# Optimization experiments

Hardware: AMD Instinct MI355X
Metric: run time of the kernel (lower is better)

## Reference

```python
import jax, jax.numpy as jnp
import numpy as np

N_NODES = 20000
N_REL = 200
DIM = 128
N_EDGES = 200000
N_TIMES = 8


def setup_inputs() -> dict:
    key = jax.random.key(0)
    ks = jax.random.split(key, 12)
    s = 1.0 / np.sqrt(DIM)
    return {
        "edge_index": jax.random.randint(ks[0], (2, N_EDGES), 0, N_NODES),
        "edge_type": jax.random.randint(ks[1], (N_EDGES,), 0, N_REL),
        "edge_time": jax.random.randint(ks[2], (N_EDGES,), 0, N_TIMES),
        "edge_weight": jax.random.uniform(ks[3], (N_EDGES,), dtype=jnp.float32),
        "node_emb": jax.random.normal(ks[4], (N_NODES, DIM), dtype=jnp.float32),
        "rel_emb": jax.random.normal(ks[5], (N_REL, DIM), dtype=jnp.float32),
        "W_enc": jax.random.normal(ks[6], (DIM, DIM), dtype=jnp.float32) * s,
        "Wz": jax.random.normal(ks[7], (DIM, DIM), dtype=jnp.float32) * s,
        "Uz": jax.random.normal(ks[8], (DIM, DIM), dtype=jnp.float32) * s,
        "Wh": jax.random.normal(ks[9], (DIM, DIM), dtype=jnp.float32) * s,
        "Uh": jax.random.normal(ks[10], (DIM, DIM), dtype=jnp.float32) * s,
        "bz": jnp.zeros((DIM,), dtype=jnp.float32),
        "bh": jnp.zeros((DIM,), dtype=jnp.float32),
        "num_times": N_TIMES,
    }


def reference(edge_index, edge_type, edge_time, edge_weight,
              node_emb, rel_emb, W_enc, Wz, Uz, Wh, Uh, bz, bh, num_times):
    # TemporalEncoder.forward: loop over sorted unique timestamps; per-step
    # masked-edge GNN encode (R-GCN lite) then gated SSM cell; state detached.
    src, dst = edge_index[0], edge_index[1]
    rel_e = rel_emb[edge_type]          # [E, D] gather (constant across steps)
    src_e = node_emb[src]               # [E, D]
    n_nodes = node_emb.shape[0]

    def step(state, t):
        m = (edge_time == t).astype(edge_weight.dtype)       # [E]
        msg = src_e * rel_e * (edge_weight * m)[:, None]     # [E, D]
        agg = jax.ops.segment_sum(msg, dst, num_segments=n_nodes)  # [N, D]
        h = jnp.tanh(agg @ W_enc)                            # base_encoder output
        z = jax.nn.sigmoid(h @ Wz + state @ Uz + bz)
        cand = jnp.tanh(h @ Wh + state @ Uh + bh)
        new_state = (1.0 - z) * state + z * cand             # ssm.cell
        return jax.lax.stop_gradient(new_state), new_state   # state.detach()

    state0 = jnp.zeros_like(node_emb)
    _, outs = jax.lax.scan(step, state0, jnp.arange(num_times))
    return outs[-1]  # last_out, shape [N, D]
```

## Files before the change

kernel.cpp:

```cpp
#include <hip/hip_runtime.h>

#define N_NODES 20000
#define N_REL 200
#define N_EDGES 200000
#define DIM 128
#define T_STEPS 8
#define N_TILES (N_NODES / 16)
#define KEYS (N_NODES * T_STEPS)
#define SCAN_N (KEYS + 1)
#define SCAN_BLKS ((SCAN_N + 1023) / 1024)

typedef short short8 __attribute__((ext_vector_type(8)));
typedef float f32x4 __attribute__((ext_vector_type(4)));

static __device__ __forceinline__ unsigned short f2bf(float f) {
  union { float f; unsigned u; } v; v.f = f;
  unsigned r = v.u + 0x7fffu + ((v.u >> 16) & 1u);
  return (unsigned short)(r >> 16);
}
static __device__ __forceinline__ unsigned cvt_pk_bf16(float lo, float hi) {
  unsigned r;
  asm("v_cvt_pk_bf16_f32 %0, %1, %2" : "=v"(r) : "v"(lo), "v"(hi));
  return r;
}
static __device__ __forceinline__ float fast_tanh(float x) {
  float e = __expf(2.f * x);
  return 1.f - 2.f / (e + 1.f);
}
static __device__ __forceinline__ float fast_sig(float x) {
  return 1.f / (1.f + __expf(-x));
}

__global__ void repack5(const float* __restrict__ w0,
                        const float* __restrict__ w1,
                        const float* __restrict__ w2,
                        const float* __restrict__ w3,
                        const float* __restrict__ w4,
                        unsigned short* __restrict__ pack) {
  int i = blockIdx.x * blockDim.x + threadIdx.x;
  if (i >= 5 * 16384) return;
  int m = i >> 14, r = i & 16383;
  int j = r & 7, lane = (r >> 3) & 63, ks = (r >> 9) & 3, nt = (r >> 11) & 7;
  int n = nt * 16 + (lane & 15);
  int k = ks * 32 + (lane >> 4) * 8 + j;
  const float* w = (m == 0) ? w0 : (m == 1) ? w1 : (m == 2) ? w2
                 : (m == 3) ? w3 : w4;
  pack[i] = f2bf(w[k * DIM + n]);
}

__global__ void hist_k(const int* __restrict__ dst, const int* __restrict__ etime,
                       int* __restrict__ counts) {
  int i = blockIdx.x * blockDim.x + threadIdx.x;
  if (i >= N_EDGES) return;
  atomicAdd(&counts[dst[i] * T_STEPS + etime[i]], 1);
}

__global__ void scan1_k(const int* __restrict__ counts,
                        int* __restrict__ base, int* __restrict__ bsum) {
  __shared__ int ls[256];
  int tid = threadIdx.x;
  int i0 = blockIdx.x * 1024 + tid * 4;
  int v[4], ts = 0;
#pragma unroll
  for (int r = 0; r < 4; r++) {
    v[r] = (i0 + r < SCAN_N) ? counts[i0 + r] : 0;
    ts += v[r];
  }
  ls[tid] = ts; __syncthreads();
#pragma unroll
  for (int off = 1; off < 256; off <<= 1) {
    int x = (tid >= off) ? ls[tid - off] : 0;
    __syncthreads(); ls[tid] += x; __syncthreads();
  }
  int run = ls[tid] - ts;
  if (tid == 255) bsum[blockIdx.x] = ls[255];
#pragma unroll
  for (int r = 0; r < 4; r++) {
    if (i0 + r < SCAN_N) base[i0 + r] = run;
    run += v[r];
  }
}

__global__ void scan2_k(int* __restrict__ bsum) {
  __shared__ int ls[256];
  int tid = threadIdx.x;
  int v = (tid < SCAN_BLKS) ? bsum[tid] : 0;
  ls[tid] = v; __syncthreads();
#pragma unroll
  for (int off = 1; off < 256; off <<= 1) {
    int x = (tid >= off) ? ls[tid - off] : 0;
    __syncthreads(); ls[tid] += x; __syncthreads();
  }
  if (tid < SCAN_BLKS) bsum[tid] = ls[tid] - v;
}

__global__ void scan3_k(int* __restrict__ base, const int* __restrict__ bsum) {
  int i = blockIdx.x * blockDim.x + threadIdx.x;
  if (i < SCAN_N) base[i] += bsum[i >> 10];
}

__global__ void fill_k(const int* __restrict__ src, const int* __restrict__ dst,
                       const int* __restrict__ etype, const int* __restrict__ etime,
                       const float* __restrict__ ew,
                       const int* __restrict__ base, int* __restrict__ cursor,
                       unsigned* __restrict__ epack, float* __restrict__ sw) {
  int i = blockIdx.x * blockDim.x + threadIdx.x;
  if (i >= N_EDGES) return;
  int key = dst[i] * T_STEPS + etime[i];
  int pos = base[key] + atomicAdd(&cursor[key], 1);
  epack[pos] = (unsigned)src[i] | ((unsigned)etype[i] << 15);
  sw[pos] = ew[i];
}

__global__ void gather_k(const int* __restrict__ base,
                         const unsigned* __restrict__ epack,
                         const float* __restrict__ sw,
                         const float* __restrict__ nemb,
                         const float* __restrict__ remb,
                         unsigned short* __restrict__ aggb) {
  int lane = threadIdx.x & 63;
  int node = (blockIdx.x * blockDim.x + threadIdx.x) >> 6;
  const int* b = base + node * T_STEPS;
  int i = b[0];
#pragma unroll
  for (int tt = 0; tt < T_STEPS; tt++) {
    int e1 = b[tt + 1];
    float ax = 0.f, ay = 0.f;
    for (; i < e1; i++) {
      unsigned u = epack[i];
      float w = sw[i];
      int s = u & 0x7fff, rt = u >> 15;
      float2 sv = ((const float2*)(nemb + (size_t)s * DIM))[lane];
      float2 rv = ((const float2*)(remb + (size_t)rt * DIM))[lane];
      ax += sv.x * rv.x * w;
      ay += sv.y * rv.y * w;
    }
    ((unsigned*)(aggb + ((size_t)tt * N_NODES + node) * DIM))[lane] =
        cvt_pk_bf16(ax, ay);
  }
}

__launch_bounds__(512, 4)
__global__ void fused_recur(const unsigned short* __restrict__ aggb,
                            const unsigned short* __restrict__ pack,
                            const float* __restrict__ bz,
                            const float* __restrict__ bh,
                            float* __restrict__ out) {
  __shared__ unsigned short Hb[2][16 * 136];
  __shared__ unsigned short Sb[2][16 * 136];
  int lane = threadIdx.x & 63;
  int nt = threadIdx.x >> 6;
  int tile = blockIdx.x;
  int q = lane >> 4, l15 = lane & 15;
  int row0 = tile * 16;

  unsigned hpk[T_STEPS][2];
  {
    short8 wenc[4];
#pragma unroll
    for (int ks = 0; ks < 4; ks++)
      wenc[ks] = *(const short8*)(pack + ((nt * 4 + ks) * 64 + lane) * 8);
#pragma unroll
    for (int t = 0; t < T_STEPS; t++) {
      f32x4 acch = (f32x4){0.f, 0.f, 0.f, 0.f};
#pragma unroll
      for (int ks = 0; ks < 4; ks++) {
        short8 aA = *(const short8*)(aggb +
            ((size_t)t * N_NODES + row0 + l15) * DIM + ks * 32 + q * 8);
        acch = __builtin_amdgcn_mfma_f32_16x16x32_bf16(aA, wenc[ks], acch, 0, 0, 0);
      }
      hpk[t][0] = cvt_pk_bf16(fast_tanh(acch[0]), fast_tanh(acch[1]));
      hpk[t][1] = cvt_pk_bf16(fast_tanh(acch[2]), fast_tanh(acch[3]));
    }
  }

  short8 wz[4], uz[4], wh[4], uh[4];
#pragma unroll
  for (int ks = 0; ks < 4; ks++) {
    int fo = ((nt * 4 + ks) * 64 + lane) * 8;
    wz[ks] = *(const short8*)(pack + 16384 * 1 + fo);
    uz[ks] = *(const short8*)(pack + 16384 * 2 + fo);
    wh[ks] = *(const short8*)(pack + 16384 * 3 + fo);
    uh[ks] = *(const short8*)(pack + 16384 * 4 + fo);
  }
  float bzv = bz[nt * 16 + l15];
  float bhv = bh[nt * 16 + l15];

  f32x4 stC = (f32x4){0.f, 0.f, 0.f, 0.f};
  int c = nt * 16 + l15;

#pragma unroll
  for (int t = 0; t < T_STEPS; t++) {
    unsigned short* hB = Hb[t & 1];
    unsigned short* sB = Sb[t & 1];
    unsigned s01 = cvt_pk_bf16(stC[0], stC[1]);
    unsigned s23 = cvt_pk_bf16(stC[2], stC[3]);
    hB[(q * 4 + 0) * 136 + c] = (unsigned short)hpk[t][0];
    hB[(q * 4 + 1) * 136 + c] = (unsigned short)(hpk[t][0] >> 16);
    hB[(q * 4 + 2) * 136 + c] = (unsigned short)hpk[t][1];
    hB[(q * 4 + 3) * 136 + c] = (unsigned short)(hpk[t][1] >> 16);
    sB[(q * 4 + 0) * 136 + c] = (unsigned short)s01;
    sB[(q * 4 + 1) * 136 + c] = (unsigned short)(s01 >> 16);
    sB[(q * 4 + 2) * 136 + c] = (unsigned short)s23;
    sB[(q * 4 + 3) * 136 + c] = (unsigned short)(s23 >> 16);
    __syncthreads();

    f32x4 accz = (f32x4){bzv, bzv, bzv, bzv};
    f32x4 accc = (f32x4){bhv, bhv, bhv, bhv};
#pragma unroll
    for (int ks = 0; ks < 4; ks++) {
      short8 hA = *(const short8*)&hB[l15 * 136 + ks * 32 + q * 8];
      short8 sA = *(const short8*)&sB[l15 * 136 + ks * 32 + q * 8];
      accz = __builtin_amdgcn_mfma_f32_16x16x32_bf16(hA, wz[ks], accz, 0, 0, 0);
      accz = __builtin_amdgcn_mfma_f32_16x16x32_bf16(sA, uz[ks], accz, 0, 0, 0);
      accc = __builtin_amdgcn_mfma_f32_16x16x32_bf16(hA, wh[ks], accc, 0, 0, 0);
      accc = __builtin_amdgcn_mfma_f32_16x16x32_bf16(sA, uh[ks], accc, 0, 0, 0);
    }
#pragma unroll
    for (int r = 0; r < 4; r++) {
      float z = fast_sig(accz[r]);
      float cc = fast_tanh(accc[r]);
      stC[r] = (1.f - z) * stC[r] + z * cc;
    }
  }

#pragma unroll
  for (int r = 0; r < 4; r++)
    out[(size_t)(row0 + q * 4 + r) * DIM + nt * 16 + l15] = stC[r];
}

extern "C" void kernel_launch(void* const* d_in, const int* in_sizes, int n_in,
                              void* d_out, int out_size, void* d_ws, size_t ws_size,
                              hipStream_t stream) {
  const int* eidx  = (const int*)d_in[0];
  const int* src   = eidx;
  const int* dst   = eidx + N_EDGES;
  const int* etype = (const int*)d_in[1];
  const int* etime = (const int*)d_in[2];
  const float* ew   = (const float*)d_in[3];
  const float* nemb = (const float*)d_in[4];
  const float* remb = (const float*)d_in[5];
  const float* Wenc = (const float*)d_in[6];
  const float* Wz   = (const float*)d_in[7];
  const float* Uz   = (const float*)d_in[8];
  const float* Wh   = (const float*)d_in[9];
  const float* Uh   = (const float*)d_in[10];
  const float* bz   = (const float*)d_in[11];
  const float* bh   = (const float*)d_in[12];

  unsigned short* aggb = (unsigned short*)d_ws;
  int* counts = (int*)(aggb + (size_t)T_STEPS * N_NODES * DIM);
  int* cursor = counts + SCAN_N;
  int* bsum   = cursor + KEYS;
  int* base   = bsum + 256;
  unsigned* epack = (unsigned*)(base + SCAN_N);
  float* sw   = (float*)(epack + N_EDGES);
  unsigned short* pack = (unsigned short*)(sw + N_EDGES);
  float* outp = (float*)d_out;

  hipMemsetAsync(counts, 0, (size_t)(SCAN_N + KEYS) * sizeof(int), stream);
  repack5<<<(5 * 16384 + 255) / 256, 256, 0, stream>>>(Wenc, Wz, Uz, Wh, Uh, pack);
  hist_k<<<(N_EDGES + 255) / 256, 256, 0, stream>>>(dst, etime, counts);
  scan1_k<<<SCAN_BLKS, 256, 0, stream>>>(counts, base, bsum);
  scan2_k<<<1, 256, 0, stream>>>(bsum);
  scan3_k<<<(SCAN_N + 255) / 256, 256, 0, stream>>>(base, bsum);
  fill_k<<<(N_EDGES + 255) / 256, 256, 0, stream>>>(src, dst, etype, etime, ew,
                                                    base, cursor, epack, sw);
  gather_k<<<N_NODES / 4, 256, 0, stream>>>(base, epack, sw, nemb, remb, aggb);
  fused_recur<<<N_TILES, 512, 0, stream>>>(aggb, pack, bz, bh, outp);
}
```

Measured before the change: 226.1 us.

## Give each wave a full node tile in recurrence; pack edge index and weight

The fused recurrence kernel now assigns one 16-row tile per wave, with each wave computing all 8 column tiles. Weights are streamed from global/L2 on every step instead of being held in registers, and state lives in registers as 8x4 floats per lane. Per-wave XOR-swizzled LDS scratch replaces the block-wide shared buffers, which removes __syncthreads, and the first step skips the state matmuls. Edge source/type and weight are packed into one uint2 so each edge needs a single load. The trade-off is repeated weight fetches and higher register pressure in exchange for no block barriers.

```diff
diff --git a/kernel.cpp b/kernel.cpp
--- a/kernel.cpp
+++ b/kernel.cpp
@@ -9,6 +9,8 @@
 #define KEYS (N_NODES * T_STEPS)
 #define SCAN_N (KEYS + 1)
 #define SCAN_BLKS ((SCAN_N + 1023) / 1024)
+#define TILE_WAVES 4
+#define FUSE_BLKS ((N_TILES + TILE_WAVES - 1) / TILE_WAVES)
 
 typedef short short8 __attribute__((ext_vector_type(8)));
 typedef float f32x4 __attribute__((ext_vector_type(4)));
@@ -103,18 +105,19 @@
                        const int* __restrict__ etype, const int* __restrict__ etime,
                        const float* __restrict__ ew,
                        const int* __restrict__ base, int* __restrict__ cursor,
-                       unsigned* __restrict__ epack, float* __restrict__ sw) {
+                       uint2* __restrict__ ep2) {
   int i = blockIdx.x * blockDim.x + threadIdx.x;
   if (i >= N_EDGES) return;
   int key = dst[i] * T_STEPS + etime[i];
   int pos = base[key] + atomicAdd(&cursor[key], 1);
-  epack[pos] = (unsigned)src[i] | ((unsigned)etype[i] << 15);
-  sw[pos] = ew[i];
+  uint2 e;
+  e.x = (unsigned)src[i] | ((unsigned)etype[i] << 15);
+  e.y = __float_as_uint(ew[i]);
+  ep2[pos] = e;
 }
 
 __global__ void gather_k(const int* __restrict__ base,
-                         const unsigned* __restrict__ epack,
-                         const float* __restrict__ sw,
+                         const uint2* __restrict__ ep2,
                          const float* __restrict__ nemb,
                          const float* __restrict__ remb,
                          unsigned short* __restrict__ aggb) {
@@ -127,9 +130,9 @@
     int e1 = b[tt + 1];
     float ax = 0.f, ay = 0.f;
     for (; i < e1; i++) {
-      unsigned u = epack[i];
-      float w = sw[i];
-      int s = u & 0x7fff, rt = u >> 15;
+      uint2 e = ep2[i];
+      float w = __uint_as_float(e.y);
+      int s = e.x & 0x7fff, rt = e.x >> 15;
       float2 sv = ((const float2*)(nemb + (size_t)s * DIM))[lane];
       float2 rv = ((const float2*)(remb + (size_t)rt * DIM))[lane];
       ax += sv.x * rv.x * w;
@@ -140,93 +143,118 @@
   }
 }
 
-__launch_bounds__(512, 4)
+__launch_bounds__(256, 2)
 __global__ void fused_recur(const unsigned short* __restrict__ aggb,
                             const unsigned short* __restrict__ pack,
                             const float* __restrict__ bz,
                             const float* __restrict__ bh,
                             float* __restrict__ out) {
-  __shared__ unsigned short Hb[2][16 * 136];
-  __shared__ unsigned short Sb[2][16 * 136];
+  __shared__ unsigned short scr[TILE_WAVES][2][16 * 128];
   int lane = threadIdx.x & 63;
-  int nt = threadIdx.x >> 6;
-  int tile = blockIdx.x;
+  int wv = threadIdx.x >> 6;
+  int tile = blockIdx.x * TILE_WAVES + wv;
+  if (tile >= N_TILES) return;
   int q = lane >> 4, l15 = lane & 15;
+  int x3 = l15 & 3;
   int row0 = tile * 16;
-
-  unsigned hpk[T_STEPS][2];
-  {
-    short8 wenc[4];
+  unsigned short* hS = &scr[wv][0][0];
+  unsigned short* sS = &scr[wv][1][0];
+
+  const unsigned short* packL = pack + (size_t)lane * 8;
+
+  float bzr[8], bhr[8];
+#pragma unroll
+  for (int nt = 0; nt < 8; nt++) {
+    bzr[nt] = bz[nt * 16 + l15];
+    bhr[nt] = bh[nt * 16 + l15];
+  }
+
+  float st[8][4];
+#pragma unroll
+  for (int nt = 0; nt < 8; nt++)
+#pragma unroll
+    for (int r = 0; r < 4; r++) st[nt][r] = 0.f;
+
+  int rb = l15 * 128 + q * 8;
+
+  for (int t = 0; t < T_STEPS; t++) {
+    short8 aggA[4];
+    const unsigned short* arow =
+        aggb + ((size_t)t * N_NODES + row0 + l15) * DIM + q * 8;
 #pragma unroll
     for (int ks = 0; ks < 4; ks++)
-      wenc[ks] = *(const short8*)(pack + ((nt * 4 + ks) * 64 + lane) * 8);
-#pragma unroll
-    for (int t = 0; t < T_STEPS; t++) {
+      aggA[ks] = *(const short8*)(arow + ks * 32);
+
+    short8 sAf[4];
+    if (t > 0) {
+#pragma unroll
+      for (int ks = 0; ks < 4; ks++)
+        sAf[ks] = *(const short8*)&sS[rb + ((ks ^ x3) << 5)];
+    }
+
+#pragma unroll
+    for (int nt = 0; nt < 8; nt++) {
       f32x4 acch = (f32x4){0.f, 0.f, 0.f, 0.f};
 #pragma unroll
       for (int ks = 0; ks < 4; ks++) {
-        short8 aA = *(const short8*)(aggb +
-            ((size_t)t * N_NODES + row0 + l15) * DIM + ks * 32 + q * 8);
-        acch = __builtin_amdgcn_mfma_f32_16x16x32_bf16(aA, wenc[ks], acch, 0, 0, 0);
-      }
-      hpk[t][0] = cvt_pk_bf16(fast_tanh(acch[0]), fast_tanh(acch[1]));
-      hpk[t][1] = cvt_pk_bf16(fast_tanh(acch[2]), fast_tanh(acch[3]));
-    }
-  }
-
-  short8 wz[4], uz[4], wh[4], uh[4];
-#pragma unroll
-  for (int ks = 0; ks < 4; ks++) {
-    int fo = ((nt * 4 + ks) * 64 + lane) * 8;
-    wz[ks] = *(const short8*)(pack + 16384 * 1 + fo);
-    uz[ks] = *(const short8*)(pack + 16384 * 2 + fo);
-    wh[ks] = *(const short8*)(pack + 16384 * 3 + fo);
-    uh[ks] = *(const short8*)(pack + 16384 * 4 + fo);
-  }
-  float bzv = bz[nt * 16 + l15];
-  float bhv = bh[nt * 16 + l15];
-
-  f32x4 stC = (f32x4){0.f, 0.f, 0.f, 0.f};
-  int c = nt * 16 + l15;
-
-#pragma unroll
-  for (int t = 0; t < T_STEPS; t++) {
-    unsigned short* hB = Hb[t & 1];
-    unsigned short* sB = Sb[t & 1];
-    unsigned s01 = cvt_pk_bf16(stC[0], stC[1]);
-    unsigned s23 = cvt_pk_bf16(stC[2], stC[3]);
-    hB[(q * 4 + 0) * 136 + c] = (unsigned short)hpk[t][0];
-    hB[(q * 4 + 1) * 136 + c] = (unsigned short)(hpk[t][0] >> 16);
-    hB[(q * 4 + 2) * 136 + c] = (unsigned short)hpk[t][1];
-    hB[(q * 4 + 3) * 136 + c] = (unsigned short)(hpk[t][1] >> 16);
-    sB[(q * 4 + 0) * 136 + c] = (unsigned short)s01;
-    sB[(q * 4 + 1) * 136 + c] = (unsigned short)(s01 >> 16);
-    sB[(q * 4 + 2) * 136 + c] = (unsigned short)s23;
-    sB[(q * 4 + 3) * 136 + c] = (unsigned short)(s23 >> 16);
-    __syncthreads();
-
-    f32x4 accz = (f32x4){bzv, bzv, bzv, bzv};
-    f32x4 accc = (f32x4){bhv, bhv, bhv, bhv};
-#pragma unroll
-    for (int ks = 0; ks < 4; ks++) {
-      short8 hA = *(const short8*)&hB[l15 * 136 + ks * 32 + q * 8];
-      short8 sA = *(const short8*)&sB[l15 * 136 + ks * 32 + q * 8];
-      accz = __builtin_amdgcn_mfma_f32_16x16x32_bf16(hA, wz[ks], accz, 0, 0, 0);
-      accz = __builtin_amdgcn_mfma_f32_16x16x32_bf16(sA, uz[ks], accz, 0, 0, 0);
-      accc = __builtin_amdgcn_mfma_f32_16x16x32_bf16(hA, wh[ks], accc, 0, 0, 0);
-      accc = __builtin_amdgcn_mfma_f32_16x16x32_bf16(sA, uh[ks], accc, 0, 0, 0);
-    }
-#pragma unroll
-    for (int r = 0; r < 4; r++) {
-      float z = fast_sig(accz[r]);
-      float cc = fast_tanh(accc[r]);
-      stC[r] = (1.f - z) * stC[r] + z * cc;
-    }
-  }
-
-#pragma unroll
-  for (int r = 0; r < 4; r++)
-    out[(size_t)(row0 + q * 4 + r) * DIM + nt * 16 + l15] = stC[r];
+        short8 wB = *(const short8*)(packL + ((nt * 4 + ks) << 9));
+        acch = __builtin_amdgcn_mfma_f32_16x16x32_bf16(aggA[ks], wB, acch, 0, 0, 0);
+      }
+      unsigned h01 = cvt_pk_bf16(fast_tanh(acch[0]), fast_tanh(acch[1]));
+      unsigned h23 = cvt_pk_bf16(fast_tanh(acch[2]), fast_tanh(acch[3]));
+      int c0 = nt * 16 + l15;
+      hS[(((q * 4 + 0) * 128 + c0) ^ (0 << 5))] = (unsigned short)h01;
+      hS[(((q * 4 + 1) * 128 + c0) ^ (1 << 5))] = (unsigned short)(h01 >> 16);
+      hS[(((q * 4 + 2) * 128 + c0) ^ (2 << 5))] = (unsigned short)h23;
+      hS[(((q * 4 + 3) * 128 + c0) ^ (3 << 5))] = (unsigned short)(h23 >> 16);
+    }
+
+    short8 hAf[4];
+#pragma unroll
+    for (int ks = 0; ks < 4; ks++)
+      hAf[ks] = *(const short8*)&hS[rb + ((ks ^ x3) << 5)];
+
+#pragma unroll
+    for (int nt = 0; nt < 8; nt++) {
+      f32x4 accz = (f32x4){bzr[nt], bzr[nt], bzr[nt], bzr[nt]};
+      f32x4 accc = (f32x4){bhr[nt], bhr[nt], bhr[nt], bhr[nt]};
+#pragma unroll
+      for (int ks = 0; ks < 4; ks++) {
+        const unsigned short* pf = packL + ((nt * 4 + ks) << 9);
+        accz = __builtin_amdgcn_mfma_f32_16x16x32_bf16(
+            hAf[ks], *(const short8*)(pf + 16384 * 1), accz, 0, 0, 0);
+        accc = __builtin_amdgcn_mfma_f32_16x16x32_bf16(
+            hAf[ks], *(const short8*)(pf + 16384 * 3), accc, 0, 0, 0);
+        if (t > 0) {
+          accz = __builtin_amdgcn_mfma_f32_16x16x32_bf16(
+              sAf[ks], *(const short8*)(pf + 16384 * 2), accz, 0, 0, 0);
+          accc = __builtin_amdgcn_mfma_f32_16x16x32_bf16(
+              sAf[ks], *(const short8*)(pf + 16384 * 4), accc, 0, 0, 0);
+        }
+      }
+#pragma unroll
+      for (int r = 0; r < 4; r++) {
+        float z = fast_sig(accz[r]);
+        float cc = fast_tanh(accc[r]);
+        st[nt][r] = (1.f - z) * st[nt][r] + z * cc;
+      }
+      if (t + 1 < T_STEPS) {
+        unsigned s01 = cvt_pk_bf16(st[nt][0], st[nt][1]);
+        unsigned s23 = cvt_pk_bf16(st[nt][2], st[nt][3]);
+        int c0 = nt * 16 + l15;
+        sS[(((q * 4 + 0) * 128 + c0) ^ (0 << 5))] = (unsigned short)s01;
+        sS[(((q * 4 + 1) * 128 + c0) ^ (1 << 5))] = (unsigned short)(s01 >> 16);
+        sS[(((q * 4 + 2) * 128 + c0) ^ (2 << 5))] = (unsigned short)s23;
+        sS[(((q * 4 + 3) * 128 + c0) ^ (3 << 5))] = (unsigned short)(s23 >> 16);
+      }
+    }
+  }
+
+#pragma unroll
+  for (int nt = 0; nt < 8; nt++)
+#pragma unroll
+    for (int r = 0; r < 4; r++)
+      out[(size_t)(row0 + q * 4 + r) * DIM + nt * 16 + l15] = st[nt][r];
 }
 
 extern "C" void kernel_launch(void* const* d_in, const int* in_sizes, int n_in,
@@ -253,9 +281,8 @@
   int* cursor = counts + SCAN_N;
   int* bsum   = cursor + KEYS;
   int* base   = bsum + 256;
-  unsigned* epack = (unsigned*)(base + SCAN_N);
-  float* sw   = (float*)(epack + N_EDGES);
-  unsigned short* pack = (unsigned short*)(sw + N_EDGES);
+  uint2* ep2  = (uint2*)(base + ((SCAN_N + 1) & ~1));
+  unsigned short* pack = (unsigned short*)(ep2 + N_EDGES);
   float* outp = (float*)d_out;
 
   hipMemsetAsync(counts, 0, (size_t)(SCAN_N + KEYS) * sizeof(int), stream);
@@ -265,7 +292,7 @@
   scan2_k<<<1, 256, 0, stream>>>(bsum);
   scan3_k<<<(SCAN_N + 255) / 256, 256, 0, stream>>>(base, bsum);
   fill_k<<<(N_EDGES + 255) / 256, 256, 0, stream>>>(src, dst, etype, etime, ew,
-                                                    base, cursor, epack, sw);
-  gather_k<<<N_NODES / 4, 256, 0, stream>>>(base, epack, sw, nemb, remb, aggb);
-  fused_recur<<<N_TILES, 512, 0, stream>>>(aggb, pack, bz, bh, outp);
-}
+                                                    base, cursor, ep2);
+  gather_k<<<N_NODES / 4, 256, 0, stream>>>(base, ep2, nemb, remb, aggb);
+  fused_recur<<<FUSE_BLKS, 256, 0, stream>>>(aggb, pack, bz, bh, outp);
+}
```

Measured after the change: 588.5 us. 160% more time.
